# Optimization experiments

Hardware: AMD Instinct MI355X
Metric: run time of the kernel (lower is better)

The kernel has to match this reference:

```python
import jax, jax.numpy as jnp
import numpy as np

SEQ_LEN = 4096
PRED_LEN = 4096
D_MODEL = 512
PERIOD = 32
N = SEQ_LEN // PERIOD   # 128
M = PRED_LEN // PERIOD  # 128
K = 2 * (PERIOD // 2) + 1  # 33
B = 32


def setup_inputs() -> dict:
    key = jax.random.key(0)
    k1, k2, k3 = jax.random.split(key, 3)
    h = jax.random.normal(k1, (B, SEQ_LEN, D_MODEL), dtype=jnp.float32)
    # torch Conv1d weight layout: [out_ch, in_ch/groups, k] = [D, 1, K]
    conv_w = jax.random.normal(k2, (D_MODEL, 1, K), dtype=jnp.float32) * (1.0 / np.sqrt(K))
    # torch Linear(n, m, bias=False) weight: [m, n]
    backbone_w = jax.random.normal(k3, (M, N), dtype=jnp.float32) * (1.0 / np.sqrt(N))
    return {"h": h, "conv_w": conv_w, "backbone_w": backbone_w}


def reference(h, conv_w, backbone_w):
    Bb, L, D = h.shape
    w, n, m, H = PERIOD, N, M, PRED_LEN
    h_t = jnp.transpose(h, (0, 2, 1))  # [B, D, L]
    conv = jax.lax.conv_general_dilated(
        h_t, conv_w,
        window_strides=(1,),
        padding=[(K // 2, K // 2)],
        dimension_numbers=("NCH", "OIH", "NCH"),
        feature_group_count=D,
    )
    h_agg = h_t + conv  # residual depthwise conv, [B, D, L]
    # rearrange into phases: [B*D, n, w] -> [B*D, w, n]
    x_by_phase = jnp.transpose(h_agg.reshape(Bb * D, n, w), (0, 2, 1))
    # per-phase linear n -> m (Linear weight is [m, n], applied as x @ W^T)
    y_by_phase = jnp.einsum("pwn,mn->pwm", x_by_phase, backbone_w)  # [B*D, w, m]
    # de-interleave phases back into a length-H sequence
    y_reordered = jnp.transpose(y_by_phase, (0, 2, 1)).reshape(Bb * D, H)
    y = jnp.transpose(y_reordered.reshape(Bb, D, H), (0, 2, 1))  # [B, H, D]
    return y
```

## Files before the change

kernel.cpp:

```cpp
#include <hip/hip_runtime.h>
#include <hip/hip_bf16.h>

#define SEQ_LEN 4096
#define D_MODEL 512
#define KSZ 33

typedef __attribute__((ext_vector_type(8))) short short8;
typedef __attribute__((ext_vector_type(4))) short short4v;
typedef __attribute__((ext_vector_type(4))) float float4v;
typedef __attribute__((ext_vector_type(4))) unsigned short ushort4v;

static __device__ __forceinline__ unsigned short f2bf(float f) {
    unsigned int u = __float_as_uint(f);
    u += 0x7fffu + ((u >> 16) & 1u);
    return (unsigned short)(u >> 16);
}

__global__ __launch_bounds__(256) void k_conv(const float* __restrict__ h,
                                              const float* __restrict__ cw,
                                              float* __restrict__ hagg) {
    __shared__ float tile[96][64];
    __shared__ float wsh[64][33];

    const int lt = blockIdx.x, dt = blockIdx.y, b = blockIdx.z;
    const int tid = threadIdx.x;
    const int c = tid & 63;
    const int l0 = lt * 64;

    const float* hb = h + ((size_t)b * SEQ_LEN) * D_MODEL + dt * 64;
    for (int r = (tid >> 6); r < 96; r += 4) {
        int l = l0 - 16 + r;
        float v = 0.f;
        if (l >= 0 && l < SEQ_LEN) v = hb[(size_t)l * D_MODEL + c];
        tile[r][c] = v;
    }
    for (int idx = tid; idx < 64 * KSZ; idx += 256) {
        int dd = idx / KSZ, k = idx - dd * KSZ;
        wsh[dd][k] = cw[(size_t)(dt * 64 + dd) * KSZ + k];
    }
    __syncthreads();

    float wreg[KSZ];
#pragma unroll
    for (int k = 0; k < KSZ; k++) wreg[k] = wsh[c][k];

    const int lsub = (tid >> 6) * 16;
    float win[48];
#pragma unroll
    for (int t = 0; t < 48; t++) win[t] = tile[lsub + t][c];

    float acc[16];
#pragma unroll
    for (int j = 0; j < 16; j++) acc[j] = win[j + 16];
#pragma unroll
    for (int k = 0; k < KSZ; k++)
#pragma unroll
        for (int j = 0; j < 16; j++)
            acc[j] += wreg[k] * win[j + k];

    float* ob = hagg + ((size_t)b * SEQ_LEN + l0 + lsub) * D_MODEL + dt * 64 + c;
#pragma unroll
    for (int j = 0; j < 16; j++) ob[(size_t)j * D_MODEL] = acc[j];
}

#define WS 136
#define XS 132

__global__ __launch_bounds__(256) void k_gemm(const float* __restrict__ w,
                                              float* __restrict__ out) {
    __shared__ unsigned short wl[128 * WS];
    __shared__ unsigned short xl[64 * XS];

    const int tid = threadIdx.x;
    const int dtile = blockIdx.x, ph = blockIdx.y, b = blockIdx.z;

#pragma unroll
    for (int it = 0; it < 16; it++) {
        int idx = it * 1024 + tid * 4;
        int row = idx >> 7, col = idx & 127;
        float4v v = *(const float4v*)(w + idx);
        ushort4v o;
        o[0] = f2bf(v[0]); o[1] = f2bf(v[1]); o[2] = f2bf(v[2]); o[3] = f2bf(v[3]);
        *(ushort4v*)(&wl[row * WS + col]) = o;
    }
    {
        const int dgrp = tid & 15;
        const int ipair = tid >> 4;
        const float* xb = out + ((size_t)b * SEQ_LEN + ph) * D_MODEL
                          + dtile * 64 + dgrp * 4;
#pragma unroll
        for (int pass = 0; pass < 4; pass++) {
            int i0 = pass * 32 + ipair * 2;
            float4v v0 = *(const float4v*)(xb + (size_t)(i0) * 32 * D_MODEL);
            float4v v1 = *(const float4v*)(xb + (size_t)(i0 + 1) * 32 * D_MODEL);
#pragma unroll
            for (int dd = 0; dd < 4; dd++) {
                unsigned int pk = (unsigned int)f2bf(v0[dd])
                                | ((unsigned int)f2bf(v1[dd]) << 16);
                *(unsigned int*)(&xl[(dgrp * 4 + dd) * XS + i0]) = pk;
            }
        }
    }
    __syncthreads();

    const int lane = tid & 63, wid = tid >> 6;
    const int q = lane >> 4, r16 = lane & 15;

    float4v acc[2][4] = {};
#pragma unroll
    for (int kb = 0; kb < 128; kb += 32) {
        short8 a[2];
#pragma unroll
        for (int mt = 0; mt < 2; mt++) {
            int row = wid * 32 + mt * 16 + r16;
            a[mt] = *(const short8*)(&wl[row * WS + kb + q * 8]);
        }
#pragma unroll
        for (int dtl = 0; dtl < 4; dtl++) {
            const unsigned short* xp = &xl[(dtl * 16 + r16) * XS + kb + q * 8];
            short4v blo = *(const short4v*)(xp);
            short4v bhi = *(const short4v*)(xp + 4);
            short8 bfrag = __builtin_shufflevector(blo, bhi, 0, 1, 2, 3, 4, 5, 6, 7);
#pragma unroll
            for (int mt = 0; mt < 2; mt++)
                acc[mt][dtl] = __builtin_amdgcn_mfma_f32_16x16x32_bf16(
                    a[mt], bfrag, acc[mt][dtl], 0, 0, 0);
        }
    }

    float* ob = out + ((size_t)b * SEQ_LEN) * D_MODEL;
#pragma unroll
    for (int mt = 0; mt < 2; mt++) {
        int mbase = wid * 32 + mt * 16 + q * 4;
#pragma unroll
        for (int r = 0; r < 4; r++) {
            int m = mbase + r;
            int hidx = m * 32 + ph;
#pragma unroll
            for (int dtl = 0; dtl < 4; dtl++) {
                int d = dtile * 64 + dtl * 16 + r16;
                ob[(size_t)hidx * D_MODEL + d] = acc[mt][dtl][r];
            }
        }
    }
}

extern "C" void kernel_launch(void* const* d_in, const int* in_sizes, int n_in,
                              void* d_out, int out_size, void* d_ws, size_t ws_size,
                              hipStream_t stream) {
    const float* h  = (const float*)d_in[0];
    const float* cw = (const float*)d_in[1];
    const float* bw = (const float*)d_in[2];
    float* out = (float*)d_out;

    k_conv<<<dim3(64, 8, 32), 256, 0, stream>>>(h, cw, out);
    k_gemm<<<dim3(8, 32, 32), 256, 0, stream>>>(bw, out);
}
```

Baseline: 733.6 us.

## Store conv output as bf16 intermediate and precompute weights in prep kernel

Adds a prep kernel that converts the backbone weight to bf16 once and transposes the conv weights so each k-slice is read coalesced. The conv kernel loads h with float4 loads, folds the residual into the centre tap, uses a sliding register window, and writes its output as bf16 staged through shared memory. This halves the intermediate traffic between conv and GEMM. The GEMM kernel reads the bf16 intermediate directly into an XOR-swizzled LDS tile and takes A fragments from global instead of LDS. The intermediate is packed into the front half of each output row and later overwritten in place, which depends on each GEMM block's reads not overlapping other blocks' writes.

```diff
diff --git a/kernel.cpp b/kernel.cpp
--- a/kernel.cpp
+++ b/kernel.cpp
@@ -1,14 +1,12 @@
 #include <hip/hip_runtime.h>
-#include <hip/hip_bf16.h>
 
 #define SEQ_LEN 4096
 #define D_MODEL 512
 #define KSZ 33
 
+typedef __attribute__((ext_vector_type(4))) float float4v;
 typedef __attribute__((ext_vector_type(8))) short short8;
-typedef __attribute__((ext_vector_type(4))) short short4v;
-typedef __attribute__((ext_vector_type(4))) float float4v;
-typedef __attribute__((ext_vector_type(4))) unsigned short ushort4v;
+typedef __attribute__((ext_vector_type(8))) unsigned short ushort8;
 
 static __device__ __forceinline__ unsigned short f2bf(float f) {
     unsigned int u = __float_as_uint(f);
@@ -16,95 +14,106 @@
     return (unsigned short)(u >> 16);
 }
 
-__global__ __launch_bounds__(256) void k_conv(const float* __restrict__ h,
+__global__ __launch_bounds__(256) void k_prep(const float* __restrict__ bw,
                                               const float* __restrict__ cw,
-                                              float* __restrict__ hagg) {
+                                              unsigned short* __restrict__ wb,
+                                              float* __restrict__ wt) {
+    int i = blockIdx.x * 256 + threadIdx.x;
+    if (i < 128 * 128) wb[i] = f2bf(bw[i]);
+    if (i < KSZ * D_MODEL) {
+        int k = i >> 9, d = i & 511;
+        wt[i] = cw[(size_t)d * KSZ + k];
+    }
+}
+
+__global__ __launch_bounds__(256, 6) void k_conv(const float* __restrict__ h,
+                                                 const float* __restrict__ wt,
+                                                 float* __restrict__ outp) {
     __shared__ float tile[96][64];
-    __shared__ float wsh[64][33];
 
     const int lt = blockIdx.x, dt = blockIdx.y, b = blockIdx.z;
     const int tid = threadIdx.x;
-    const int c = tid & 63;
     const int l0 = lt * 64;
 
     const float* hb = h + ((size_t)b * SEQ_LEN) * D_MODEL + dt * 64;
-    for (int r = (tid >> 6); r < 96; r += 4) {
-        int l = l0 - 16 + r;
-        float v = 0.f;
-        if (l >= 0 && l < SEQ_LEN) v = hb[(size_t)l * D_MODEL + c];
-        tile[r][c] = v;
-    }
-    for (int idx = tid; idx < 64 * KSZ; idx += 256) {
-        int dd = idx / KSZ, k = idx - dd * KSZ;
-        wsh[dd][k] = cw[(size_t)(dt * 64 + dd) * KSZ + k];
-    }
-    __syncthreads();
-
-    float wreg[KSZ];
+    {
+        const int cg = (tid & 15) * 4;
 #pragma unroll
-    for (int k = 0; k < KSZ; k++) wreg[k] = wsh[c][k];
-
-    const int lsub = (tid >> 6) * 16;
-    float win[48];
-#pragma unroll
-    for (int t = 0; t < 48; t++) win[t] = tile[lsub + t][c];
-
-    float acc[16];
-#pragma unroll
-    for (int j = 0; j < 16; j++) acc[j] = win[j + 16];
-#pragma unroll
-    for (int k = 0; k < KSZ; k++)
-#pragma unroll
-        for (int j = 0; j < 16; j++)
-            acc[j] += wreg[k] * win[j + k];
-
-    float* ob = hagg + ((size_t)b * SEQ_LEN + l0 + lsub) * D_MODEL + dt * 64 + c;
-#pragma unroll
-    for (int j = 0; j < 16; j++) ob[(size_t)j * D_MODEL] = acc[j];
-}
-
-#define WS 136
-#define XS 132
-
-__global__ __launch_bounds__(256) void k_gemm(const float* __restrict__ w,
-                                              float* __restrict__ out) {
-    __shared__ unsigned short wl[128 * WS];
-    __shared__ unsigned short xl[64 * XS];
-
-    const int tid = threadIdx.x;
-    const int dtile = blockIdx.x, ph = blockIdx.y, b = blockIdx.z;
-
-#pragma unroll
-    for (int it = 0; it < 16; it++) {
-        int idx = it * 1024 + tid * 4;
-        int row = idx >> 7, col = idx & 127;
-        float4v v = *(const float4v*)(w + idx);
-        ushort4v o;
-        o[0] = f2bf(v[0]); o[1] = f2bf(v[1]); o[2] = f2bf(v[2]); o[3] = f2bf(v[3]);
-        *(ushort4v*)(&wl[row * WS + col]) = o;
-    }
-    {
-        const int dgrp = tid & 15;
-        const int ipair = tid >> 4;
-        const float* xb = out + ((size_t)b * SEQ_LEN + ph) * D_MODEL
-                          + dtile * 64 + dgrp * 4;
-#pragma unroll
-        for (int pass = 0; pass < 4; pass++) {
-            int i0 = pass * 32 + ipair * 2;
-            float4v v0 = *(const float4v*)(xb + (size_t)(i0) * 32 * D_MODEL);
-            float4v v1 = *(const float4v*)(xb + (size_t)(i0 + 1) * 32 * D_MODEL);
-#pragma unroll
-            for (int dd = 0; dd < 4; dd++) {
-                unsigned int pk = (unsigned int)f2bf(v0[dd])
-                                | ((unsigned int)f2bf(v1[dd]) << 16);
-                *(unsigned int*)(&xl[(dgrp * 4 + dd) * XS + i0]) = pk;
-            }
+        for (int rr = 0; rr < 6; rr++) {
+            int r = (tid >> 4) + rr * 16;
+            int l = l0 - 16 + r;
+            float4v v = {0.f, 0.f, 0.f, 0.f};
+            if (l >= 0 && l < SEQ_LEN) v = *(const float4v*)(hb + (size_t)l * D_MODEL + cg);
+            *(float4v*)(&tile[r][cg]) = v;
         }
     }
     __syncthreads();
 
-    const int lane = tid & 63, wid = tid >> 6;
-    const int q = lane >> 4, r16 = lane & 15;
+    const int c = tid & 63;
+    const int lsub = (tid >> 6) * 16;
+    const float* wcol = wt + dt * 64 + c;
+
+    float buf[16];
+#pragma unroll
+    for (int j = 0; j < 16; j++) buf[j] = tile[lsub + j][c];
+    float acc[16] = {};
+#pragma unroll
+    for (int k = 0; k < KSZ; k++) {
+        float wk = wcol[(size_t)k * D_MODEL] + ((k == 16) ? 1.0f : 0.0f);
+#pragma unroll
+        for (int j = 0; j < 16; j++) acc[j] += wk * buf[j];
+        if (k < 32) {
+#pragma unroll
+            for (int j = 0; j < 15; j++) buf[j] = buf[j + 1];
+            buf[15] = tile[lsub + k + 16][c];
+        }
+    }
+    __syncthreads();
+
+    unsigned short* ot = (unsigned short*)&tile[0][0];
+#pragma unroll
+    for (int j = 0; j < 16; j++) ot[(lsub + j) * 64 + c] = f2bf(acc[j]);
+    __syncthreads();
+#pragma unroll
+    for (int p = 0; p < 2; p++) {
+        int idx = tid + p * 256;
+        int row = idx >> 3, cg = idx & 7;
+        ushort8 v = *(const ushort8*)(&ot[row * 64 + cg * 8]);
+        char* dst = (char*)outp + ((size_t)(b * SEQ_LEN + l0 + row) * 2048) + dt * 256 + cg * 16;
+        *(ushort8*)dst = v;
+    }
+}
+
+#define XS 136
+__global__ __launch_bounds__(256, 4) void k_gemm(const unsigned short* __restrict__ wb,
+                                                 float* __restrict__ outp) {
+    __shared__ unsigned short xl[64 * XS];
+
+    const int tid = threadIdx.x;
+    const int dt = blockIdx.x, ph = blockIdx.y, b = blockIdx.z;
+
+    const char* xbase = (const char*)outp
+                      + ((size_t)(b * SEQ_LEN + ph) * D_MODEL + dt * 64) * 4;
+#pragma unroll
+    for (int p = 0; p < 2; p++) {
+        int idx = tid + p * 256;
+        int pr = idx >> 3;
+        int cg = idx & 7;
+        const char* src = xbase + (size_t)(2 * pr) * (32 * 2048) + cg * 16;
+        ushort8 r0 = *(const ushort8*)(src);
+        ushort8 r1 = *(const ushort8*)(src + 32 * 2048);
+        int B = pr >> 2;
+        int wof = (2 * pr) & 7;
+#pragma unroll
+        for (int dd = 0; dd < 8; dd++) {
+            int d = cg * 8 + dd;
+            unsigned int pk = (unsigned int)r0[dd] | ((unsigned int)r1[dd] << 16);
+            *(unsigned int*)(&xl[d * XS + ((B ^ cg) << 3) + wof]) = pk;
+        }
+    }
+    __syncthreads();
+
+    const int lane = tid & 63, wid = tid >> 6, q = lane >> 4, r16 = lane & 15;
 
     float4v acc[2][4] = {};
 #pragma unroll
@@ -113,14 +122,13 @@
 #pragma unroll
         for (int mt = 0; mt < 2; mt++) {
             int row = wid * 32 + mt * 16 + r16;
-            a[mt] = *(const short8*)(&wl[row * WS + kb + q * 8]);
+            a[mt] = *(const short8*)(wb + row * 128 + kb + q * 8);
         }
 #pragma unroll
         for (int dtl = 0; dtl < 4; dtl++) {
-            const unsigned short* xp = &xl[(dtl * 16 + r16) * XS + kb + q * 8];
-            short4v blo = *(const short4v*)(xp);
-            short4v bhi = *(const short4v*)(xp + 4);
-            short8 bfrag = __builtin_shufflevector(blo, bhi, 0, 1, 2, 3, 4, 5, 6, 7);
+            int d = dtl * 16 + r16;
+            int Bb = ((kb >> 3) + q) ^ (d >> 3);
+            short8 bfrag = *(const short8*)(&xl[d * XS + (Bb << 3)]);
 #pragma unroll
             for (int mt = 0; mt < 2; mt++)
                 acc[mt][dtl] = __builtin_amdgcn_mfma_f32_16x16x32_bf16(
@@ -128,7 +136,7 @@
         }
     }
 
-    float* ob = out + ((size_t)b * SEQ_LEN) * D_MODEL;
+    float* ob = outp + ((size_t)b * SEQ_LEN) * D_MODEL;
 #pragma unroll
     for (int mt = 0; mt < 2; mt++) {
         int mbase = wid * 32 + mt * 16 + q * 4;
@@ -138,7 +146,7 @@
             int hidx = m * 32 + ph;
 #pragma unroll
             for (int dtl = 0; dtl < 4; dtl++) {
-                int d = dtile * 64 + dtl * 16 + r16;
+                int d = dt * 64 + dtl * 16 + r16;
                 ob[(size_t)hidx * D_MODEL + d] = acc[mt][dtl][r];
             }
         }
@@ -153,6 +161,10 @@
     const float* bw = (const float*)d_in[2];
     float* out = (float*)d_out;
 
-    k_conv<<<dim3(64, 8, 32), 256, 0, stream>>>(h, cw, out);
-    k_gemm<<<dim3(8, 32, 32), 256, 0, stream>>>(bw, out);
+    unsigned short* wb = (unsigned short*)d_ws;
+    float* wt = (float*)((char*)d_ws + 32768);
+
+    k_prep<<<dim3(66), 256, 0, stream>>>(bw, cw, wb, wt);
+    k_conv<<<dim3(64, 8, 32), 256, 0, stream>>>(h, wt, out);
+    k_gemm<<<dim3(8, 32, 32), 256, 0, stream>>>(wb, out);
 }
```

After: 945.6 us. 28.9% more time.
